# Kernel optimization log

Hardware: AMD Instinct MI355X
Metric: run time of the kernel (lower is better)

## Reference

```python
import jax, jax.numpy as jnp
import numpy as np

B, T, S, F, H, V = 4, 160, 80, 640, 1024, 1024

def setup_inputs() -> dict:
    key = jax.random.key(0)
    ks = jax.random.split(key, 4)
    return {
        "source_encodings": jax.random.normal(ks[0], (B, T, F), dtype=jnp.float32),
        "target_encodings": jax.random.normal(ks[1], (B, S, F), dtype=jnp.float32),
        "W1": jax.random.normal(ks[2], (F, H), dtype=jnp.float32) * (1.0 / np.sqrt(F)),
        "b1": jnp.zeros((H,), dtype=jnp.float32),
        "W2": jax.random.normal(ks[3], (H, V), dtype=jnp.float32) * (1.0 / np.sqrt(H)),
        "b2": jnp.zeros((V,), dtype=jnp.float32),
    }

def reference(source_encodings, target_encodings, W1, b1, W2, b2):
    # broadcast add: [B,T,1,F] + [B,1,S,F] -> [B,T,S,F]
    combined = source_encodings[:, :, None, :] + target_encodings[:, None, :, :]
    # FFN: Linear -> ReLU -> Linear (dropout=0 / eval)
    h = jax.nn.relu(jnp.einsum("btsf,fh->btsh", combined, W1) + b1)
    logits = jnp.einsum("btsh,hv->btsv", h, W2) + b2
    # eval mode applies log_softmax over vocab
    return jax.nn.log_softmax(logits, axis=-1)
```

## Files before the change

### kernel.cpp

```cpp
#include <hip/hip_runtime.h>
#include <type_traits>
#include <utility>

#define B_ 4
#define T_ 160
#define S_ 80
#define F_ 640
#define H_ 1024
#define V_ 1024

typedef float f32x4 __attribute__((ext_vector_type(4)));
typedef short s16x8 __attribute__((ext_vector_type(8)));
typedef __bf16 bf16x8_t __attribute__((ext_vector_type(8)));

template <typename T, typename = void>
struct MfmaTakes : std::false_type {};
template <typename T>
struct MfmaTakes<T, std::void_t<decltype(__builtin_amdgcn_mfma_f32_16x16x32_bf16(
    std::declval<T>(), std::declval<T>(), std::declval<f32x4>(), 0, 0, 0))>>
    : std::true_type {};

template <typename S8>
__device__ __forceinline__ f32x4 mfma_bf16_16x16x32(S8 a, S8 b, f32x4 c) {
  if constexpr (MfmaTakes<S8>::value) {
    return __builtin_amdgcn_mfma_f32_16x16x32_bf16(a, b, c, 0, 0, 0);
  } else {
    return __builtin_amdgcn_mfma_f32_16x16x32_bf16(
        __builtin_bit_cast(bf16x8_t, a), __builtin_bit_cast(bf16x8_t, b), c, 0, 0, 0);
  }
}

__device__ __forceinline__ unsigned short f2bf(float x) {
  unsigned int u = __float_as_uint(x);
  u += 0x7FFFu + ((u >> 16) & 1u);
  return (unsigned short)(u >> 16);
}

__global__ __launch_bounds__(256) void prep_weights(const float* __restrict__ W1,
                                                    const float* __restrict__ W2,
                                                    s16x8* __restrict__ W1p,
                                                    s16x8* __restrict__ W2p) {
  const int NW1 = (F_ / 8) * H_;
  const int NW2 = (H_ / 8) * V_;
  int c = blockIdx.x * 256 + threadIdx.x;
  if (c < NW1) {
    int kg = c >> 10, v = c & 1023;
    s16x8 o;
#pragma unroll
    for (int i = 0; i < 8; ++i) o[i] = (short)f2bf(W1[(kg * 8 + i) * H_ + v]);
    W1p[c] = o;
  } else if (c < NW1 + NW2) {
    int c2 = c - NW1;
    int kg = c2 >> 10, v = c2 & 1023;
    s16x8 o;
#pragma unroll
    for (int i = 0; i < 8; ++i) o[i] = (short)f2bf(W2[(kg * 8 + i) * V_ + v]);
    W2p[c2] = o;
  }
}

__global__ __launch_bounds__(512, 2) void pq_gemm(const float* __restrict__ src,
                                                  const float* __restrict__ tgt,
                                                  const s16x8* __restrict__ W1p,
                                                  const float* __restrict__ b1,
                                                  float* __restrict__ P,
                                                  float* __restrict__ Q) {
  __shared__ s16x8 a_lds[64 * 80];
  const int tid = threadIdx.x;
  const int wr = blockIdx.x;
  const int r0 = wr * 64;
  const bool isP = (wr < 10);

  for (int c = tid; c < 64 * 80; c += 512) {
    int m = c / 80, kg8 = c - m * 80;
    int R = r0 + m;
    const float* rowp = isP ? (src + R * F_) : (tgt + (R - 640) * F_);
    const f32x4* p4 = (const f32x4*)(rowp + kg8 * 8);
    f32x4 x0 = p4[0], x1 = p4[1];
    s16x8 o;
#pragma unroll
    for (int i = 0; i < 4; ++i) o[i] = (short)f2bf(x0[i]);
#pragma unroll
    for (int i = 0; i < 4; ++i) o[4 + i] = (short)f2bf(x1[i]);
    a_lds[m * 80 + (kg8 ^ (m & 7))] = o;
  }
  __syncthreads();

  const int l = tid & 63, wv = tid >> 6;
  const int g = l >> 4, cl = l & 15;
  const f32x4 zero = {0.f, 0.f, 0.f, 0.f};
  f32x4 acc[4][8];
#pragma unroll
  for (int rt = 0; rt < 4; ++rt)
#pragma unroll
    for (int ct = 0; ct < 8; ++ct) acc[rt][ct] = zero;

  const s16x8* bbase = W1p + g * 1024 + wv * 128 + cl;
  s16x8 bA[8], bB[8], af[4];
#pragma unroll
  for (int ct = 0; ct < 8; ++ct) bA[ct] = bbase[ct * 16];

  for (int ks = 0; ks < 20; ks += 2) {
#pragma unroll
    for (int ct = 0; ct < 8; ++ct) bB[ct] = bbase[(ks + 1) * 4096 + ct * 16];
#pragma unroll
    for (int rt = 0; rt < 4; ++rt) {
      int m = rt * 16 + cl;
      af[rt] = a_lds[m * 80 + ((ks * 4 + g) ^ (m & 7))];
    }
#pragma unroll
    for (int ct = 0; ct < 8; ++ct)
#pragma unroll
      for (int rt = 0; rt < 4; ++rt)
        acc[rt][ct] = mfma_bf16_16x16x32(af[rt], bA[ct], acc[rt][ct]);
    int ksn = (ks + 2 < 20) ? (ks + 2) : 0;
#pragma unroll
    for (int ct = 0; ct < 8; ++ct) bA[ct] = bbase[ksn * 4096 + ct * 16];
#pragma unroll
    for (int rt = 0; rt < 4; ++rt) {
      int m = rt * 16 + cl;
      af[rt] = a_lds[m * 80 + (((ks + 1) * 4 + g) ^ (m & 7))];
    }
#pragma unroll
    for (int ct = 0; ct < 8; ++ct)
#pragma unroll
      for (int rt = 0; rt < 4; ++rt)
        acc[rt][ct] = mfma_bf16_16x16x32(af[rt], bB[ct], acc[rt][ct]);
  }

  float b1v[8];
#pragma unroll
  for (int ct = 0; ct < 8; ++ct) b1v[ct] = isP ? b1[wv * 128 + ct * 16 + cl] : 0.f;
  float* outbase = isP ? P : Q;
  const int orow0 = isP ? r0 : (r0 - 640);
#pragma unroll
  for (int rt = 0; rt < 4; ++rt) {
#pragma unroll
    for (int j = 0; j < 4; ++j) {
      int row = rt * 16 + g * 4 + j;
      float* op = outbase + (size_t)(orow0 + row) * H_ + wv * 128 + cl;
#pragma unroll
      for (int ct = 0; ct < 8; ++ct) op[ct * 16] = acc[rt][ct][j] + b1v[ct];
    }
  }
}

__global__ __launch_bounds__(1024, 4) void joint_main(const float* __restrict__ Pm,
                                                      const float* __restrict__ Qm,
                                                      const s16x8* __restrict__ W2p,
                                                      const float* __restrict__ b2,
                                                      float* __restrict__ out) {
  __shared__ s16x8 h_lds[64 * 128];
  const int tid = threadIdx.x;
  int bx = blockIdx.x;
  int bid = (bx & 7) * 100 + (bx >> 3);
  const int b = bid / 200;
  int rem = bid - b * 200;
  const int t0 = (rem / 10) * 8;
  const int s0 = (rem - (rem / 10) * 10) * 8;

  for (int c = tid; c < 64 * 128; c += 1024) {
    int m = c >> 7, kg8 = c & 127;
    int dt = m >> 3, ds = m & 7;
    const f32x4* p4 = (const f32x4*)(Pm + (size_t)(b * T_ + t0 + dt) * H_ + kg8 * 8);
    const f32x4* q4 = (const f32x4*)(Qm + (size_t)(b * S_ + s0 + ds) * H_ + kg8 * 8);
    f32x4 x0 = p4[0] + q4[0];
    f32x4 x1 = p4[1] + q4[1];
    s16x8 o;
#pragma unroll
    for (int i = 0; i < 4; ++i) o[i] = (short)f2bf(fmaxf(x0[i], 0.f));
#pragma unroll
    for (int i = 0; i < 4; ++i) o[4 + i] = (short)f2bf(fmaxf(x1[i], 0.f));
    h_lds[m * 128 + (kg8 ^ (m & 7))] = o;
  }
  __syncthreads();

  const int l = tid & 63, wv = tid >> 6;
  const int g = l >> 4, cl = l & 15;
  const f32x4 zero = {0.f, 0.f, 0.f, 0.f};
  f32x4 acc[4][4];
#pragma unroll
  for (int rt = 0; rt < 4; ++rt)
#pragma unroll
    for (int ct = 0; ct < 4; ++ct) acc[rt][ct] = zero;

  const s16x8* bbase = W2p + g * 1024 + wv * 64 + cl;

#pragma unroll 2
  for (int ks = 0; ks < 32; ++ks) {
    s16x8 b0 = bbase[ks * 4096];
    s16x8 b1f = bbase[ks * 4096 + 16];
    s16x8 b2f = bbase[ks * 4096 + 32];
    s16x8 b3f = bbase[ks * 4096 + 48];
    int m0 = cl, m1 = 16 + cl, m2 = 32 + cl, m3 = 48 + cl;
    int kc = ks * 4 + g;
    s16x8 a0 = h_lds[m0 * 128 + (kc ^ (m0 & 7))];
    s16x8 a1 = h_lds[m1 * 128 + (kc ^ (m1 & 7))];
    s16x8 a2 = h_lds[m2 * 128 + (kc ^ (m2 & 7))];
    s16x8 a3 = h_lds[m3 * 128 + (kc ^ (m3 & 7))];
    acc[0][0] = mfma_bf16_16x16x32(a0, b0, acc[0][0]);
    acc[1][0] = mfma_bf16_16x16x32(a1, b0, acc[1][0]);
    acc[2][0] = mfma_bf16_16x16x32(a2, b0, acc[2][0]);
    acc[3][0] = mfma_bf16_16x16x32(a3, b0, acc[3][0]);
    acc[0][1] = mfma_bf16_16x16x32(a0, b1f, acc[0][1]);
    acc[1][1] = mfma_bf16_16x16x32(a1, b1f, acc[1][1]);
    acc[2][1] = mfma_bf16_16x16x32(a2, b1f, acc[2][1]);
    acc[3][1] = mfma_bf16_16x16x32(a3, b1f, acc[3][1]);
    acc[0][2] = mfma_bf16_16x16x32(a0, b2f, acc[0][2]);
    acc[1][2] = mfma_bf16_16x16x32(a1, b2f, acc[1][2]);
    acc[2][2] = mfma_bf16_16x16x32(a2, b2f, acc[2][2]);
    acc[3][2] = mfma_bf16_16x16x32(a3, b2f, acc[3][2]);
    acc[0][3] = mfma_bf16_16x16x32(a0, b3f, acc[0][3]);
    acc[1][3] = mfma_bf16_16x16x32(a1, b3f, acc[1][3]);
    acc[2][3] = mfma_bf16_16x16x32(a2, b3f, acc[2][3]);
    acc[3][3] = mfma_bf16_16x16x32(a3, b3f, acc[3][3]);
  }

  __syncthreads();
  float* redm = reinterpret_cast<float*>(h_lds);
  float* reds = redm + 1024;
  float* lsebuf = reds + 1024;

#pragma unroll
  for (int ct = 0; ct < 4; ++ct) {
    float bv = b2[wv * 64 + ct * 16 + cl];
#pragma unroll
    for (int rt = 0; rt < 4; ++rt)
#pragma unroll
      for (int j = 0; j < 4; ++j) acc[rt][ct][j] += bv;
  }

#pragma unroll
  for (int rt = 0; rt < 4; ++rt)
#pragma unroll
    for (int j = 0; j < 4; ++j) {
      float mx = fmaxf(fmaxf(acc[rt][0][j], acc[rt][1][j]),
                       fmaxf(acc[rt][2][j], acc[rt][3][j]));
#pragma unroll
      for (int msk = 1; msk < 16; msk <<= 1) mx = fmaxf(mx, __shfl_xor(mx, msk, 64));
      if (cl == 0) redm[wv * 64 + rt * 16 + g * 4 + j] = mx;
    }
  __syncthreads();

#pragma unroll
  for (int rt = 0; rt < 4; ++rt)
#pragma unroll
    for (int j = 0; j < 4; ++j) {
      int row = rt * 16 + g * 4 + j;
      float gm = redm[row];
#pragma unroll
      for (int w = 1; w < 16; ++w) gm = fmaxf(gm, redm[w * 64 + row]);
      float ps = __expf(acc[rt][0][j] - gm) + __expf(acc[rt][1][j] - gm) +
                 __expf(acc[rt][2][j] - gm) + __expf(acc[rt][3][j] - gm);
#pragma unroll
      for (int msk = 1; msk < 16; msk <<= 1) ps += __shfl_xor(ps, msk, 64);
      if (cl == 0) reds[wv * 64 + rt * 16 + g * 4 + j] = ps;
    }
  __syncthreads();

  if (tid < 64) {
    int row = tid;
    float gm = redm[row], s = 0.f;
#pragma unroll
    for (int w = 1; w < 16; ++w) gm = fmaxf(gm, redm[w * 64 + row]);
#pragma unroll
    for (int w = 0; w < 16; ++w) s += reds[w * 64 + row];
    lsebuf[row] = gm + __logf(s);
  }
  __syncthreads();

#pragma unroll
  for (int rt = 0; rt < 4; ++rt)
#pragma unroll
    for (int j = 0; j < 4; ++j) {
      int row = rt * 16 + g * 4 + j;
      float lse = lsebuf[row];
      int n = (b * T_ + t0 + (row >> 3)) * S_ + s0 + (row & 7);
      float* op = out + (size_t)n * V_ + wv * 64 + cl;
#pragma unroll
      for (int ct = 0; ct < 4; ++ct) op[ct * 16] = acc[rt][ct][j] - lse;
    }
}

extern "C" void kernel_launch(void* const* d_in, const int* in_sizes, int n_in,
                              void* d_out, int out_size, void* d_ws, size_t ws_size,
                              hipStream_t stream) {
  const float* src = (const float*)d_in[0];
  const float* tgt = (const float*)d_in[1];
  const float* W1  = (const float*)d_in[2];
  const float* b1  = (const float*)d_in[3];
  const float* W2  = (const float*)d_in[4];
  const float* b2  = (const float*)d_in[5];
  float* out = (float*)d_out;

  char* ws = (char*)d_ws;
  s16x8* W1p = (s16x8*)(ws);
  s16x8* W2p = (s16x8*)(ws + 1310720);
  float* P   = (float*)(ws + 3407872);
  float* Q   = (float*)(ws + 6029312);

  prep_weights<<<832, 256, 0, stream>>>(W1, W2, W1p, W2p);
  pq_gemm<<<15, 512, 0, stream>>>(src, tgt, W1p, b1, P, Q);
  joint_main<<<800, 1024, 0, stream>>>(P, Q, W2p, b2, out);
}
```

Measured before the change: 220.9 us.

## Switch second GEMM to 32x32x16 MFMA with register-prefetched W2 fragments

The second GEMM's inner loop moves from 16x16x32 bf16 MFMA tiles (4x4 accumulators) to 32x32x16 tiles (2x2 f32x16 accumulators). W2 fragments for the next k-step are loaded one iteration ahead to hide global-load latency. The log-softmax reduction is reorganised to match the new accumulator layout: the row max is reduced once into a shared buffer and reused, and partial sums are handled as vector lanes. The aim is fewer MFMA issues and fewer LDS reads of A fragments per FLOP, at the cost of higher register pressure from prefetching and the larger accumulators.

```diff
diff --git a/kernel.cpp b/kernel.cpp
--- a/kernel.cpp
+++ b/kernel.cpp
@@ -10,6 +10,7 @@
 #define V_ 1024
 
 typedef float f32x4 __attribute__((ext_vector_type(4)));
+typedef float f32x16 __attribute__((ext_vector_type(16)));
 typedef short s16x8 __attribute__((ext_vector_type(8)));
 typedef __bf16 bf16x8_t __attribute__((ext_vector_type(8)));
 
@@ -26,6 +27,23 @@
     return __builtin_amdgcn_mfma_f32_16x16x32_bf16(a, b, c, 0, 0, 0);
   } else {
     return __builtin_amdgcn_mfma_f32_16x16x32_bf16(
+        __builtin_bit_cast(bf16x8_t, a), __builtin_bit_cast(bf16x8_t, b), c, 0, 0, 0);
+  }
+}
+
+template <typename T, typename = void>
+struct Mfma32Takes : std::false_type {};
+template <typename T>
+struct Mfma32Takes<T, std::void_t<decltype(__builtin_amdgcn_mfma_f32_32x32x16_bf16(
+    std::declval<T>(), std::declval<T>(), std::declval<f32x16>(), 0, 0, 0))>>
+    : std::true_type {};
+
+template <typename S8>
+__device__ __forceinline__ f32x16 mfma_bf16_32x32x16(S8 a, S8 b, f32x16 c) {
+  if constexpr (Mfma32Takes<S8>::value) {
+    return __builtin_amdgcn_mfma_f32_32x32x16_bf16(a, b, c, 0, 0, 0);
+  } else {
+    return __builtin_amdgcn_mfma_f32_32x32x16_bf16(
         __builtin_bit_cast(bf16x8_t, a), __builtin_bit_cast(bf16x8_t, b), c, 0, 0, 0);
   }
 }
@@ -176,110 +194,129 @@
   __syncthreads();
 
   const int l = tid & 63, wv = tid >> 6;
-  const int g = l >> 4, cl = l & 15;
-  const f32x4 zero = {0.f, 0.f, 0.f, 0.f};
-  f32x4 acc[4][4];
-#pragma unroll
-  for (int rt = 0; rt < 4; ++rt)
-#pragma unroll
-    for (int ct = 0; ct < 4; ++ct) acc[rt][ct] = zero;
-
-  const s16x8* bbase = W2p + g * 1024 + wv * 64 + cl;
-
-#pragma unroll 2
-  for (int ks = 0; ks < 32; ++ks) {
-    s16x8 b0 = bbase[ks * 4096];
-    s16x8 b1f = bbase[ks * 4096 + 16];
-    s16x8 b2f = bbase[ks * 4096 + 32];
-    s16x8 b3f = bbase[ks * 4096 + 48];
-    int m0 = cl, m1 = 16 + cl, m2 = 32 + cl, m3 = 48 + cl;
-    int kc = ks * 4 + g;
-    s16x8 a0 = h_lds[m0 * 128 + (kc ^ (m0 & 7))];
-    s16x8 a1 = h_lds[m1 * 128 + (kc ^ (m1 & 7))];
-    s16x8 a2 = h_lds[m2 * 128 + (kc ^ (m2 & 7))];
-    s16x8 a3 = h_lds[m3 * 128 + (kc ^ (m3 & 7))];
-    acc[0][0] = mfma_bf16_16x16x32(a0, b0, acc[0][0]);
-    acc[1][0] = mfma_bf16_16x16x32(a1, b0, acc[1][0]);
-    acc[2][0] = mfma_bf16_16x16x32(a2, b0, acc[2][0]);
-    acc[3][0] = mfma_bf16_16x16x32(a3, b0, acc[3][0]);
-    acc[0][1] = mfma_bf16_16x16x32(a0, b1f, acc[0][1]);
-    acc[1][1] = mfma_bf16_16x16x32(a1, b1f, acc[1][1]);
-    acc[2][1] = mfma_bf16_16x16x32(a2, b1f, acc[2][1]);
-    acc[3][1] = mfma_bf16_16x16x32(a3, b1f, acc[3][1]);
-    acc[0][2] = mfma_bf16_16x16x32(a0, b2f, acc[0][2]);
-    acc[1][2] = mfma_bf16_16x16x32(a1, b2f, acc[1][2]);
-    acc[2][2] = mfma_bf16_16x16x32(a2, b2f, acc[2][2]);
-    acc[3][2] = mfma_bf16_16x16x32(a3, b2f, acc[3][2]);
-    acc[0][3] = mfma_bf16_16x16x32(a0, b3f, acc[0][3]);
-    acc[1][3] = mfma_bf16_16x16x32(a1, b3f, acc[1][3]);
-    acc[2][3] = mfma_bf16_16x16x32(a2, b3f, acc[2][3]);
-    acc[3][3] = mfma_bf16_16x16x32(a3, b3f, acc[3][3]);
+  const int c32 = l & 31, hf = l >> 5;
+  const int sw0 = c32 & 7;
+
+  f32x16 acc00 = {}, acc01 = {}, acc10 = {}, acc11 = {};
+
+  const s16x8* wb = W2p + hf * 1024 + wv * 64 + c32;
+  const s16x8* ha0 = h_lds + c32 * 128;
+  const s16x8* ha1 = h_lds + (32 + c32) * 128;
+
+  s16x8 bA0 = wb[0], bA1 = wb[32];
+  s16x8 bB0 = wb[2048], bB1 = wb[2048 + 32];
+  for (int ks = 0; ks < 64; ks += 2) {
+    int i2 = (ks + 2 < 64) ? ks + 2 : 0;
+    int i3 = (ks + 3 < 64) ? ks + 3 : 0;
+    s16x8 nA0 = wb[i2 * 2048], nA1 = wb[i2 * 2048 + 32];
+    s16x8 nB0 = wb[i3 * 2048], nB1 = wb[i3 * 2048 + 32];
+    int k0 = (ks * 2 + hf) ^ sw0;
+    s16x8 a0 = ha0[k0], a1 = ha1[k0];
+    acc00 = mfma_bf16_32x32x16(a0, bA0, acc00);
+    acc10 = mfma_bf16_32x32x16(a1, bA0, acc10);
+    acc01 = mfma_bf16_32x32x16(a0, bA1, acc01);
+    acc11 = mfma_bf16_32x32x16(a1, bA1, acc11);
+    int k1 = k0 ^ 2;
+    s16x8 c0 = ha0[k1], c1 = ha1[k1];
+    acc00 = mfma_bf16_32x32x16(c0, bB0, acc00);
+    acc10 = mfma_bf16_32x32x16(c1, bB0, acc10);
+    acc01 = mfma_bf16_32x32x16(c0, bB1, acc01);
+    acc11 = mfma_bf16_32x32x16(c1, bB1, acc11);
+    bA0 = nA0; bA1 = nA1; bB0 = nB0; bB1 = nB1;
   }
 
   __syncthreads();
   float* redm = reinterpret_cast<float*>(h_lds);
-  float* reds = redm + 1024;
+  float* gmbuf = redm + 1024;
+  float* reds = gmbuf + 64;
   float* lsebuf = reds + 1024;
 
-#pragma unroll
-  for (int ct = 0; ct < 4; ++ct) {
-    float bv = b2[wv * 64 + ct * 16 + cl];
-#pragma unroll
-    for (int rt = 0; rt < 4; ++rt)
-#pragma unroll
-      for (int j = 0; j < 4; ++j) acc[rt][ct][j] += bv;
-  }
-
-#pragma unroll
-  for (int rt = 0; rt < 4; ++rt)
-#pragma unroll
-    for (int j = 0; j < 4; ++j) {
-      float mx = fmaxf(fmaxf(acc[rt][0][j], acc[rt][1][j]),
-                       fmaxf(acc[rt][2][j], acc[rt][3][j]));
-#pragma unroll
-      for (int msk = 1; msk < 16; msk <<= 1) mx = fmaxf(mx, __shfl_xor(mx, msk, 64));
-      if (cl == 0) redm[wv * 64 + rt * 16 + g * 4 + j] = mx;
-    }
-  __syncthreads();
-
-#pragma unroll
-  for (int rt = 0; rt < 4; ++rt)
-#pragma unroll
-    for (int j = 0; j < 4; ++j) {
-      int row = rt * 16 + g * 4 + j;
-      float gm = redm[row];
-#pragma unroll
-      for (int w = 1; w < 16; ++w) gm = fmaxf(gm, redm[w * 64 + row]);
-      float ps = __expf(acc[rt][0][j] - gm) + __expf(acc[rt][1][j] - gm) +
-                 __expf(acc[rt][2][j] - gm) + __expf(acc[rt][3][j] - gm);
-#pragma unroll
-      for (int msk = 1; msk < 16; msk <<= 1) ps += __shfl_xor(ps, msk, 64);
-      if (cl == 0) reds[wv * 64 + rt * 16 + g * 4 + j] = ps;
-    }
+  const float bv0 = b2[wv * 64 + c32];
+  const float bv1 = b2[wv * 64 + 32 + c32];
+#pragma unroll
+  for (int r = 0; r < 16; ++r) {
+    acc00[r] += bv0; acc10[r] += bv0;
+    acc01[r] += bv1; acc11[r] += bv1;
+  }
+
+#pragma unroll
+  for (int r = 0; r < 16; ++r) {
+    float m0 = fmaxf(acc00[r], acc01[r]);
+    float m1 = fmaxf(acc10[r], acc11[r]);
+#pragma unroll
+    for (int msk = 1; msk < 32; msk <<= 1) {
+      m0 = fmaxf(m0, __shfl_xor(m0, msk, 64));
+      m1 = fmaxf(m1, __shfl_xor(m1, msk, 64));
+    }
+    if (c32 == 0) {
+      int rr = (r & 3) + 8 * (r >> 2) + 4 * hf;
+      redm[wv * 64 + rr] = m0;
+      redm[wv * 64 + 32 + rr] = m1;
+    }
+  }
   __syncthreads();
 
   if (tid < 64) {
-    int row = tid;
-    float gm = redm[row], s = 0.f;
-#pragma unroll
-    for (int w = 1; w < 16; ++w) gm = fmaxf(gm, redm[w * 64 + row]);
-#pragma unroll
-    for (int w = 0; w < 16; ++w) s += reds[w * 64 + row];
-    lsebuf[row] = gm + __logf(s);
-  }
-  __syncthreads();
-
-#pragma unroll
-  for (int rt = 0; rt < 4; ++rt)
-#pragma unroll
-    for (int j = 0; j < 4; ++j) {
-      int row = rt * 16 + g * 4 + j;
-      float lse = lsebuf[row];
-      int n = (b * T_ + t0 + (row >> 3)) * S_ + s0 + (row & 7);
-      float* op = out + (size_t)n * V_ + wv * 64 + cl;
-#pragma unroll
-      for (int ct = 0; ct < 4; ++ct) op[ct * 16] = acc[rt][ct][j] - lse;
-    }
+    float mx = redm[tid];
+#pragma unroll
+    for (int w = 1; w < 16; ++w) mx = fmaxf(mx, redm[w * 64 + tid]);
+    gmbuf[tid] = mx;
+  }
+  __syncthreads();
+
+#pragma unroll
+  for (int rt = 0; rt < 2; ++rt) {
+#pragma unroll
+    for (int q = 0; q < 4; ++q) {
+      int rowb = rt * 32 + 8 * q + 4 * hf;
+      f32x4 gm4 = *(const f32x4*)&gmbuf[rowb];
+      f32x4 ps;
+#pragma unroll
+      for (int j = 0; j < 4; ++j) {
+        int r = q * 4 + j;
+        float e0 = (rt == 0) ? __expf(acc00[r] - gm4[j]) + __expf(acc01[r] - gm4[j])
+                             : __expf(acc10[r] - gm4[j]) + __expf(acc11[r] - gm4[j]);
+        ps[j] = e0;
+      }
+#pragma unroll
+      for (int msk = 1; msk < 32; msk <<= 1) {
+#pragma unroll
+        for (int j = 0; j < 4; ++j) ps[j] += __shfl_xor(ps[j], msk, 64);
+      }
+      if (c32 == 0) *(f32x4*)&reds[wv * 64 + rowb] = ps;
+    }
+  }
+  __syncthreads();
+
+  if (tid < 64) {
+    float s = reds[tid];
+#pragma unroll
+    for (int w = 1; w < 16; ++w) s += reds[w * 64 + tid];
+    lsebuf[tid] = gmbuf[tid] + __logf(s);
+  }
+  __syncthreads();
+
+#pragma unroll
+  for (int rt = 0; rt < 2; ++rt) {
+#pragma unroll
+    for (int q = 0; q < 4; ++q) {
+      int rowb = rt * 32 + 8 * q + 4 * hf;
+      f32x4 lse4 = *(const f32x4*)&lsebuf[rowb];
+      int n0 = (b * T_ + t0 + rt * 4 + q) * S_ + s0 + 4 * hf;
+#pragma unroll
+      for (int j = 0; j < 4; ++j) {
+        int r = q * 4 + j;
+        float* op = out + (size_t)(n0 + j) * V_ + wv * 64 + c32;
+        if (rt == 0) {
+          op[0] = acc00[r] - lse4[j];
+          op[32] = acc01[r] - lse4[j];
+        } else {
+          op[0] = acc10[r] - lse4[j];
+          op[32] = acc11[r] - lse4[j];
+        }
+      }
+    }
+  }
 }
 
 extern "C" void kernel_launch(void* const* d_in, const int* in_sizes, int n_in,
```

New measurement: 273.1 us. 23.7% more time.
